# Kernel tuning notes

Hardware: AMD Instinct MI355X
Metric: run time of the kernel (lower is better)

Reference implementation:

```python
import jax, jax.numpy as jnp
import numpy as np

B, N, DIN, DOUT, T, R, H = 4, 384, 128, 128, 4, 4, 8
DK = DOUT // H
SQRT_DK = float(np.sqrt(DK))


def setup_inputs() -> dict:
    key = jax.random.key(0)
    k = jax.random.split(key, 12)
    node_features = jax.random.normal(k[0], (B, N, DIN), jnp.float32)
    nt = jax.random.uniform(k[1], (B, N, T), dtype=jnp.float32)
    node_types_soft = nt / nt.sum(-1, keepdims=True)  # soft type distribution
    adj_matrix_soft = jax.random.uniform(k[2], (B, N, N), dtype=jnp.float32)
    et = jax.random.uniform(k[3], (B, N, N, R), dtype=jnp.float32)
    edge_types_soft = et / et.sum(-1, keepdims=True)  # soft relation distribution
    s = 0.05  # ~xavier scale for 128x128
    return dict(
        node_features=node_features,
        node_types_soft=node_types_soft,
        adj_matrix_soft=adj_matrix_soft,
        edge_types_soft=edge_types_soft,
        kw=jax.random.normal(k[4], (T, DIN, DOUT), jnp.float32) * s,
        kb=jnp.zeros((T, DOUT), jnp.float32),
        qw=jax.random.normal(k[5], (T, DIN, DOUT), jnp.float32) * s,
        qb=jnp.zeros((T, DOUT), jnp.float32),
        vw=jax.random.normal(k[6], (T, DIN, DOUT), jnp.float32) * s,
        vb=jnp.zeros((T, DOUT), jnp.float32),
        aw=jax.random.normal(k[7], (T, DOUT, DOUT), jnp.float32) * s,
        ab=jnp.zeros((T, DOUT), jnp.float32),
        norm_w=jnp.ones((T, DOUT), jnp.float32),
        norm_b=jnp.zeros((T, DOUT), jnp.float32),
        rel_pri=jnp.ones((R, H), jnp.float32),
        rel_att=jax.random.normal(k[8], (R, H, DK, DK), jnp.float32) * 0.1,
        rel_msg=jax.random.normal(k[9], (R, H, DK, DK), jnp.float32) * 0.1,
        skip=jnp.ones((T,), jnp.float32),
    )


def _forward(node_features, node_types_soft, adj_matrix_soft, edge_types_soft,
             kw, kb, qw, qb, vw, vb, aw, ab, norm_w, norm_b,
             rel_pri, rel_att, rel_msg, skip):
    Bq, Nn, _ = node_features.shape
    nt = node_types_soft
    # per-type Q/K/V projections: [B,N,T,H,DK]
    q = (jnp.einsum('bni,tid->bntd', node_features, qw) + qb).reshape(Bq, Nn, T, H, DK)
    kk = (jnp.einsum('bni,tid->bntd', node_features, kw) + kb).reshape(Bq, Nn, T, H, DK)
    v = (jnp.einsum('bni,tid->bntd', node_features, vw) + vb).reshape(Bq, Nn, T, H, DK)

    res_att = jnp.zeros((Bq, Nn, Nn, H), node_features.dtype)
    res_msg = jnp.zeros((Bq, Nn, Nn, H, DK), node_features.dtype)
    for r in range(R):  # small fixed relation count; types/heads fully vectorized
        kr = jnp.einsum('bjshe,hed->bjshd', kk, rel_att[r])
        vr = jnp.einsum('bjshe,hed->bjshd', v, rel_msg[r])
        # fold target-type mask (applied at node j in the original) into k: [B,N,Tt,Ts,H,DK]
        krt = kr[:, :, None] * nt[:, :, :, None, None, None]
        # P[b,i,j,s,h] = sum_{t,d} q[b,i,t,h,d] * nt[b,j,t] * kr[b,j,s,h,d], scaled
        P = jnp.einsum('bithd,bjtshd->bijsh', q, krt) * (rel_pri[r] / SQRT_DK)
        mask = edge_types_soft[..., r] * adj_matrix_soft  # [B,N,N]
        res_att = res_att + jnp.einsum('bijsh,bis->bijh', P, nt) * mask[..., None]
        res_msg = res_msg + jnp.einsum('bijsh,bis,bjshd->bijhd', P, nt, vr) * mask[..., None, None]

    att_sum = res_att.sum(axis=1, keepdims=True)
    safe = jnp.where(att_sum > 1e-6, att_sum, jnp.ones_like(att_sum))
    attw = (res_att / safe) * (att_sum > 1e-6).astype(res_att.dtype)
    agg = jnp.einsum('btsh,btshd->bthd', attw, res_msg).reshape(Bq, Nn, DOUT)

    trans = jnp.einsum('bnd,tdo->bnto', agg, aw) + ab
    trans = jax.nn.gelu(trans, approximate=False)  # dropout = identity at eval
    alpha = jax.nn.sigmoid(skip)[None, None, :, None]
    # in_dim == out_dim -> identity skip projection
    res = trans * alpha + node_features[:, :, None, :] * (1.0 - alpha)
    mean = res.mean(-1, keepdims=True)
    var = res.var(-1, keepdims=True)
    res = (res - mean) / jnp.sqrt(var + 1e-5) * norm_w + norm_b
    return (res * nt[..., None]).sum(axis=2)  # [B,N,DOUT]


def reference(node_features, node_types_soft, adj_matrix_soft, edge_types_soft,
              kw, kb, qw, qb, vw, vb, aw, ab, norm_w, norm_b,
              rel_pri, rel_att, rel_msg, skip):
    return _forward(node_features, node_types_soft, adj_matrix_soft, edge_types_soft,
                    kw, kb, qw, qb, vw, vb, aw, ab, norm_w, norm_b,
                    rel_pri, rel_att, rel_msg, skip)
```

## Files before the change

kernel.cpp:

```cpp
#include <hip/hip_runtime.h>
#include <math.h>

#define Bq 4
#define Nn 384
#define NB 1536
#define TT 4
#define RR 4
#define HH 8
#define DKk 16
#define APART 12288

typedef __attribute__((ext_vector_type(8))) short short8;
typedef __attribute__((ext_vector_type(4))) float f32x4;

__device__ __forceinline__ unsigned short f2bf(float f) {
  unsigned u = __float_as_uint(f);
  u += 0x7FFFu + ((u >> 16) & 1u);
  return (unsigned short)(u >> 16);
}

__device__ __forceinline__ void ld16(const float* __restrict__ p, float* o) {
  const float4* p4 = reinterpret_cast<const float4*>(p);
  float4 a = p4[0], b = p4[1], c = p4[2], d = p4[3];
  o[0]=a.x; o[1]=a.y; o[2]=a.z; o[3]=a.w;
  o[4]=b.x; o[5]=b.y; o[6]=b.z; o[7]=b.w;
  o[8]=c.x; o[9]=c.y; o[10]=c.z; o[11]=c.w;
  o[12]=d.x; o[13]=d.y; o[14]=d.z; o[15]=d.w;
}

__device__ __forceinline__ void bar_lds() {
  asm volatile("s_waitcnt lgkmcnt(0)" ::: "memory");
  __builtin_amdgcn_s_barrier();
}


__global__ __launch_bounds__(256) void k1a_qkv(
    const float* __restrict__ nf,
    const float* __restrict__ qw, const float* __restrict__ qb,
    const float* __restrict__ kw, const float* __restrict__ kb,
    const float* __restrict__ vw, const float* __restrict__ vb,
    float* __restrict__ q_ws, float* __restrict__ kv_k, float* __restrict__ kv_v)
{
  __shared__ float A_s[32][72];
  __shared__ float W_s[32][132];
  int mt = blockIdx.x, t = blockIdx.y, z = blockIdx.z;
  const float* W    = (z == 0) ? qw : ((z == 1) ? kw : vw);
  const float* bias = (z == 0) ? qb : ((z == 1) ? kb : vb);
  int tid = threadIdx.x;
  int colq = (tid & 31)*4, n8 = (tid >> 5)*8;
  float acc[8][4];
#pragma unroll
  for (int u = 0; u < 8; ++u)
#pragma unroll
    for (int c = 0; c < 4; ++c) acc[u][c] = 0.f;

  for (int kc = 0; kc < 4; ++kc) {
    __syncthreads();
    {
      int kk = tid & 31, nb0 = tid >> 5;
#pragma unroll
      for (int u = 0; u < 8; ++u)
        A_s[kk][nb0 + u*8] = nf[(size_t)(mt*64 + nb0 + u*8)*128 + kc*32 + kk];
#pragma unroll
      for (int u = 0; u < 4; ++u) {
        int idx = u*256 + tid;
        int wk = idx >> 5, c4 = (idx & 31)*4;
        *(float4*)&W_s[wk][c4] = *(const float4*)&W[(size_t)(t*128 + kc*32 + wk)*128 + c4];
      }
    }
    __syncthreads();
#pragma unroll
    for (int k = 0; k < 32; ++k) {
      float4 w4 = *(float4*)&W_s[k][colq];
      float a0[8];
      *(float4*)&a0[0] = *(float4*)&A_s[k][n8];
      *(float4*)&a0[4] = *(float4*)&A_s[k][n8 + 4];
#pragma unroll
      for (int u = 0; u < 8; ++u) {
        acc[u][0] += a0[u]*w4.x; acc[u][1] += a0[u]*w4.y;
        acc[u][2] += a0[u]*w4.z; acc[u][3] += a0[u]*w4.w;
      }
    }
  }
  float4 bv = *(const float4*)&bias[t*128 + colq];
#pragma unroll
  for (int u = 0; u < 8; ++u) {
    int node = mt*64 + n8 + u;
    float4 o;
    o.x = acc[u][0] + bv.x; o.y = acc[u][1] + bv.y;
    o.z = acc[u][2] + bv.z; o.w = acc[u][3] + bv.w;
    if (z == 0) {
      int h = colq >> 4, d = colq & 15;
      *(float4*)&q_ws[((size_t)h*NB + node)*64 + t*16 + d] = o;
    } else {
      float* dst = (z == 1) ? kv_k : kv_v;
      *(float4*)&dst[(size_t)node*512 + t*128 + colq] = o;
    }
  }
}

__global__ __launch_bounds__(256) void k1b_rel(
    const float* __restrict__ kv_k, const float* __restrict__ kv_v,
    const float* __restrict__ rel_att, const float* __restrict__ rel_msg,
    float* __restrict__ kr_ws, float* __restrict__ vr_ws,
    float* __restrict__ agg, float* __restrict__ out)
{
  __shared__ float ra_s[4][16][16];
  __shared__ float rm_s[4][16][16];
  __shared__ float k_s[16][4][17];
  __shared__ float v_s[16][4][17];
  int nb = blockIdx.x, h = blockIdx.y;
  int n0 = nb*16;
  int tid = threadIdx.x;
  agg[(size_t)(n0 + (tid >> 4))*128 + h*16 + (tid & 15)] = 0.f;
  out[(size_t)(n0 + (tid >> 4))*128 + h*16 + (tid & 15)] = 0.f;
#pragma unroll
  for (int u0 = 0; u0 < 4; ++u0) {
    int u = u0*256 + tid;
    int r = u >> 8, e = (u >> 4) & 15, d = u & 15;
    ra_s[r][e][d] = rel_att[((size_t)(r*8 + h)*16 + e)*16 + d];
    rm_s[r][e][d] = rel_msg[((size_t)(r*8 + h)*16 + e)*16 + d];
    int nl = u >> 6, s = (u >> 4) & 3, e2 = u & 15;
    k_s[nl][s][e2] = kv_k[(size_t)(n0 + nl)*512 + s*128 + h*16 + e2];
    v_s[nl][s][e2] = kv_v[(size_t)(n0 + nl)*512 + s*128 + h*16 + e2];
  }
  __syncthreads();
  int nl = tid >> 4, dq = tid & 15;
  size_t obase = ((size_t)h*NB + n0 + nl)*256;
#pragma unroll
  for (int r = 0; r < 4; ++r)
#pragma unroll
    for (int s = 0; s < 4; ++s) {
      float aK = 0.f, aV = 0.f;
#pragma unroll
      for (int e = 0; e < 16; ++e) {
        aK += k_s[nl][s][e] * ra_s[r][e][dq];
        aV += v_s[nl][s][e] * rm_s[r][e][dq];
      }
      kr_ws[obase + r*64 + s*16 + dq] = aK;
      vr_ws[obase + r*64 + s*16 + dq] = aV;
    }
}

__global__ __launch_bounds__(256,2) void k2_att(
    const float* __restrict__ nt, const float* __restrict__ adj,
    const float* __restrict__ ets, const float* __restrict__ rel_pri,
    const float* __restrict__ q_ws, const float* __restrict__ kr_ws,
    float* __restrict__ res_att, float* __restrict__ att_part)
{
  __shared__ float q_s[16*68];
  __shared__ float kr_s[32*260];
  __shared__ float ntj_s[32*4];
  int bx = blockIdx.x, h = blockIdx.y, b = blockIdx.z;
  int it = bx >> 1, jh = bx & 1;
  int i0 = it*16;
  int tid = threadIdx.x;
  int j_l = tid>>3, ig = (tid>>1)&3, dh = tid&1;
  {
    int i = tid>>4, f = (tid&15)*4;
    float4 qv = *(const float4*)&q_ws[((size_t)(h*NB) + b*Nn + i0 + i)*64 + f];
    *(float4*)&q_s[i*68 + f] = qv;
  }
  float ntiv[4][4];
#pragma unroll
  for (int il = 0; il < 4; ++il) {
    float4 v = *(const float4*)&nt[(size_t)(b*Nn + i0 + ig*4 + il)*TT];
    ntiv[il][0]=v.x; ntiv[il][1]=v.y; ntiv[il][2]=v.z; ntiv[il][3]=v.w;
  }
  float crr[4];
#pragma unroll
  for (int r = 0; r < 4; ++r) crr[r] = rel_pri[r*HH+h]*0.25f;

  for (int jc = jh*6; jc < jh*6 + 6; ++jc) {
    __syncthreads();
    {
      int js = tid>>3, gb = tid&7;
      const float* src = &kr_ws[((size_t)(h*NB) + b*Nn + jc*32 + js)*256];
      float* dst = &kr_s[js*260];
#pragma unroll
      for (int gl = 0; gl < 8; ++gl) {
        int g = gl*8 + gb;
        *(float4*)&dst[g*4] = *(const float4*)&src[g*4];
      }
      if (tid < 128) ntj_s[tid] = nt[(size_t)(b*Nn + jc*32 + (tid>>2))*TT + (tid&3)];
    }
    __syncthreads();
    int j = jc*32 + j_l;
    float nt0 = ntj_s[j_l*4+0], nt1 = ntj_s[j_l*4+1];
    float nt2 = ntj_s[j_l*4+2], nt3 = ntj_s[j_l*4+3];
    float qn[4][8];
#pragma unroll
    for (int il = 0; il < 4; ++il) {
      const float* qb2 = &q_s[(ig*4 + il)*68 + dh*8];
      float4 a0 = *(const float4*)&qb2[0],  a1 = *(const float4*)&qb2[4];
      float4 b0 = *(const float4*)&qb2[16], b1 = *(const float4*)&qb2[20];
      float4 c0 = *(const float4*)&qb2[32], c1 = *(const float4*)&qb2[36];
      float4 d0v = *(const float4*)&qb2[48], d1v = *(const float4*)&qb2[52];
      qn[il][0] = a0.x*nt0 + b0.x*nt1 + c0.x*nt2 + d0v.x*nt3;
      qn[il][1] = a0.y*nt0 + b0.y*nt1 + c0.y*nt2 + d0v.y*nt3;
      qn[il][2] = a0.z*nt0 + b0.z*nt1 + c0.z*nt2 + d0v.z*nt3;
      qn[il][3] = a0.w*nt0 + b0.w*nt1 + c0.w*nt2 + d0v.w*nt3;
      qn[il][4] = a1.x*nt0 + b1.x*nt1 + c1.x*nt2 + d1v.x*nt3;
      qn[il][5] = a1.y*nt0 + b1.y*nt1 + c1.y*nt2 + d1v.y*nt3;
      qn[il][6] = a1.z*nt0 + b1.z*nt1 + c1.z*nt2 + d1v.z*nt3;
      qn[il][7] = a1.w*nt0 + b1.w*nt1 + c1.w*nt2 + d1v.w*nt3;
    }
    float mar[4][4];
#pragma unroll
    for (int il = 0; il < 4; ++il) {
      int i = i0 + ig*4 + il;
      float a = adj[((size_t)b*Nn + i)*Nn + j];
      float4 e4 = *(const float4*)&ets[(((size_t)b*Nn + i)*Nn + j)*RR];
      mar[il][0]=e4.x*a; mar[il][1]=e4.y*a; mar[il][2]=e4.z*a; mar[il][3]=e4.w*a;
    }
    float acc[4] = {0.f,0.f,0.f,0.f};
    const float* kbp = &kr_s[j_l*260 + dh*8];
#pragma unroll
    for (int r = 0; r < 4; ++r) {
      float mr0 = mar[0][r]*crr[r], mr1 = mar[1][r]*crr[r];
      float mr2 = mar[2][r]*crr[r], mr3 = mar[3][r]*crr[r];
#pragma unroll
      for (int s = 0; s < 4; ++s) {
        float kk[8];
        *(float4*)&kk[0] = *(const float4*)&kbp[r*64 + s*16];
        *(float4*)&kk[4] = *(const float4*)&kbp[r*64 + s*16 + 4];
        float d0=0,d1=0,d2=0,d3=0;
#pragma unroll
        for (int dp = 0; dp < 8; ++dp) {
          d0 += qn[0][dp]*kk[dp]; d1 += qn[1][dp]*kk[dp];
          d2 += qn[2][dp]*kk[dp]; d3 += qn[3][dp]*kk[dp];
        }
        acc[0] += mr0*ntiv[0][s]*d0;
        acc[1] += mr1*ntiv[1][s]*d1;
        acc[2] += mr2*ntiv[2][s]*d2;
        acc[3] += mr3*ntiv[3][s]*d3;
      }
    }
#pragma unroll
    for (int il = 0; il < 4; ++il)
      acc[il] += __shfl_xor(acc[il], 1);
    if (dh == 0) {
#pragma unroll
      for (int il = 0; il < 4; ++il)
        res_att[((size_t)(b*HH + h)*Nn + i0 + ig*4 + il)*Nn + j] = acc[il];
    }
    float v = acc[0] + acc[1] + acc[2] + acc[3];
    v += __shfl_xor(v, 2);
    v += __shfl_xor(v, 4);
    if ((tid & 7) == 0)
      att_part[(size_t)it*APART + (size_t)(b*HH + h)*Nn + j] = v;
  }
}

__global__ __launch_bounds__(256) void kc_agg(
    const float* __restrict__ nt, const float* __restrict__ adj,
    const float* __restrict__ ets, const float* __restrict__ rel_pri,
    const float* __restrict__ q_ws, const float* __restrict__ kr_ws,
    const float* __restrict__ vr_ws, const float* __restrict__ res_att,
    const float* __restrict__ att_part, float* __restrict__ agg)
{
  __shared__ __align__(16) unsigned short B_lds[4][64*72];
  __shared__ __align__(16) unsigned short vr_lds[64*72];
  __shared__ __align__(16) unsigned short Z_lds[4][16*72];
  __shared__ float ntj_s[256];
  __shared__ float inv_s[64];
  int it = blockIdx.x, jc = blockIdx.y, bh = blockIdx.z;
  int b = bh >> 3, h = bh & 7;
  int tid = threadIdx.x, w = tid >> 6, l = tid & 63;
  int j0 = jc*64;
  int ib = it*64 + w*16;
  int irow = ib + (l & 15);
  int iz = ib + ((l >> 4) << 2);
  int lq = (l >> 4) * 8;
  ntj_s[tid] = nt[(size_t)(b*Nn + j0 + (tid>>2))*4 + (tid&3)];
  if (tid < 64) {
    float s = 0.f;
#pragma unroll
    for (int p = 0; p < 24; ++p)
      s += att_part[(size_t)p*APART + (size_t)bh*Nn + j0 + tid];
    inv_s[tid] = (s > 1e-6f) ? 1.f/s : 0.f;
  }
  short8 af[4][2];
  {
    float q0[8], q1[8];
    const float* qp = &q_ws[((size_t)h*NB + b*Nn + irow)*64];
    *(float4*)&q0[0] = *(const float4*)&qp[lq];
    *(float4*)&q0[4] = *(const float4*)&qp[lq + 4];
    *(float4*)&q1[0] = *(const float4*)&qp[32 + lq];
    *(float4*)&q1[4] = *(const float4*)&qp[32 + lq + 4];
    float4 ntiv = *(const float4*)&nt[(size_t)(b*Nn + irow)*4];
    float nta[4] = {ntiv.x, ntiv.y, ntiv.z, ntiv.w};
#pragma unroll
    for (int s = 0; s < 4; ++s)
#pragma unroll
      for (int e = 0; e < 8; ++e) {
        af[s][0][e] = (short)f2bf(q0[e]*nta[s]);
        af[s][1][e] = (short)f2bf(q1[e]*nta[s]);
      }
  }
  float crv[4];
#pragma unroll
  for (int r = 0; r < 4; ++r) crv[r] = rel_pri[r*HH + h]*0.25f;
  float cw[4][4];
  int eo[4][4];
  const float* ebase = ets + (size_t)b*Nn*Nn*4;
#pragma unroll
  for (int tj = 0; tj < 4; ++tj) {
    int j = j0 + tj*16 + (l & 15);
#pragma unroll
    for (int p = 0; p < 4; ++p) {
      int i = iz + p;
      cw[tj][p] = res_att[((size_t)bh*Nn + i)*Nn + j]
                * adj[((size_t)b*Nn + i)*Nn + j];
      eo[tj][p] = (i*Nn + j)*4;
    }
  }
  f32x4 agg_acc = {0.f,0.f,0.f,0.f};
  int js = tid >> 2, ss = tid & 3;
  const float* krp = &kr_ws[((size_t)h*NB + b*Nn + j0 + js)*256 + ss*16];
  const float* vrp = &vr_ws[((size_t)h*NB + b*Nn + j0 + js)*256 + ss*16];
  float kvA[16], vvA[16];
  ld16(krp, kvA);
  ld16(vrp, vvA);
  bar_lds();
#pragma unroll
  for (int tj = 0; tj < 4; ++tj) {
    float inv = inv_s[tj*16 + (l & 15)];
#pragma unroll
    for (int p = 0; p < 4; ++p) cw[tj][p] *= inv;
  }

#pragma unroll
  for (int r = 0; r < 4; ++r) {
    if (r) bar_lds();
    {
      float crr = crv[r];
      float4 ntjv = *(const float4*)&ntj_s[js*4];
      float nta[4] = {ntjv.x*crr, ntjv.y*crr, ntjv.z*crr, ntjv.w*crr};
#pragma unroll
      for (int t = 0; t < 4; ++t) {
#pragma unroll
        for (int dq = 0; dq < 2; ++dq) {
          short8 v;
#pragma unroll
          for (int e = 0; e < 8; ++e) v[e] = (short)f2bf(kvA[dq*8 + e]*nta[t]);
          *(short8*)&B_lds[ss][js*72 + t*16 + dq*8] = v;
        }
      }
#pragma unroll
      for (int d = 0; d < 16; ++d)
        vr_lds[(ss*16 + d)*72 + js] = f2bf(vvA[d]);
    }
    float kvB[16], vvB[16];
    if (r < 3) {
      ld16(krp + (r+1)*64, kvB);
      ld16(vrp + (r+1)*64, vvB);
    }
    bar_lds();
    float coef[4][4];
#pragma unroll
    for (int tj = 0; tj < 4; ++tj)
#pragma unroll
      for (int p = 0; p < 4; ++p)
        coef[tj][p] = ebase[eo[tj][p] + r] * cw[tj][p];
#pragma unroll
    for (int s = 0; s < 4; ++s) {
      f32x4 wacc[4];
#pragma unroll
      for (int tj = 0; tj < 4; ++tj) wacc[tj] = (f32x4){0.f,0.f,0.f,0.f};
#pragma unroll
      for (int tj = 0; tj < 4; ++tj) {
        short8 b0 = *(const short8*)&B_lds[s][(tj*16 + (l & 15))*72 + lq];
        short8 b1 = *(const short8*)&B_lds[s][(tj*16 + (l & 15))*72 + 32 + lq];
        wacc[tj] = __builtin_amdgcn_mfma_f32_16x16x32_bf16(af[s][0], b0, wacc[tj], 0, 0, 0);
        wacc[tj] = __builtin_amdgcn_mfma_f32_16x16x32_bf16(af[s][1], b1, wacc[tj], 0, 0, 0);
      }
#pragma unroll
      for (int tj = 0; tj < 4; ++tj)
#pragma unroll
        for (int p = 0; p < 4; ++p)
          Z_lds[w][(((l >> 4)*4) + p)*72 + tj*16 + (l & 15)] = f2bf(wacc[tj][p]*coef[tj][p]);
#pragma unroll
      for (int kj = 0; kj < 2; ++kj) {
        short8 zf = *(const short8*)&Z_lds[w][(l & 15)*72 + kj*32 + lq];
        short8 vf = *(const short8*)&vr_lds[(s*16 + (l & 15))*72 + kj*32 + lq];
        agg_acc = __builtin_amdgcn_mfma_f32_16x16x32_bf16(zf, vf, agg_acc, 0, 0, 0);
      }
    }
    if (r < 3) {
#pragma unroll
      for (int e = 0; e < 16; ++e) { kvA[e] = kvB[e]; vvA[e] = vvB[e]; }
    }
  }
#pragma unroll
  for (int p = 0; p < 4; ++p)
    atomicAdd(&agg[((size_t)b*Nn + iz + p)*128 + h*16 + (l & 15)], agg_acc[p]);
}

__global__ __launch_bounds__(128) void k5_out(
    const float* __restrict__ agg_ws, const float* __restrict__ nf,
    const float* __restrict__ nt, const float* __restrict__ aw,
    const float* __restrict__ ab, const float* __restrict__ norm_w,
    const float* __restrict__ norm_b, const float* __restrict__ skip,
    float* __restrict__ out)
{
  __shared__ float agg_s[4][128];
  int nq = blockIdx.x, t = blockIdx.y;
  int tid = threadIdx.x;
  int g = tid >> 5, o0 = (tid & 31)*4;
  {
    int nl = tid >> 5, c = (tid & 31)*4;
    *(float4*)&agg_s[nl][c] = *(const float4*)&agg_ws[(size_t)(nq*4 + nl)*128 + c];
  }
  __syncthreads();
  size_t node = (size_t)nq*4 + g;
  float alpha = 1.f/(1.f + expf(-skip[t]));
  float4 bv = *(const float4*)&ab[t*128 + o0];
  float a0 = bv.x, a1 = bv.y, a2 = bv.z, a3 = bv.w;
  const float* awt = aw + (size_t)t*128*128;
  for (int dd = 0; dd < 128; ++dd) {
    float av = agg_s[g][dd];
    float4 wv = *(const float4*)&awt[dd*128 + o0];
    a0 += av*wv.x; a1 += av*wv.y; a2 += av*wv.z; a3 += av*wv.w;
  }
  float4 nfv = *(const float4*)&nf[node*128 + o0];
  float av4[4] = {a0, a1, a2, a3};
  float nfa[4] = {nfv.x, nfv.y, nfv.z, nfv.w};
  float res[4];
#pragma unroll
  for (int c = 0; c < 4; ++c) {
    float gl = 0.5f*av4[c]*(1.f + erff(av4[c]*0.70710678118654752f));
    res[c] = gl*alpha + nfa[c]*(1.f - alpha);
  }
  float s1 = res[0]+res[1]+res[2]+res[3];
  float s2 = res[0]*res[0]+res[1]*res[1]+res[2]*res[2]+res[3]*res[3];
#pragma unroll
  for (int m = 16; m >= 1; m >>= 1) { s1 += __shfl_xor(s1, m); s2 += __shfl_xor(s2, m); }
  float mean = s1*(1.f/128.f);
  float var  = s2*(1.f/128.f) - mean*mean;
  float rstd = rsqrtf(var + 1e-5f);
  float ntv = nt[node*TT + t];
  float4 nwv = *(const float4*)&norm_w[t*128 + o0];
  float4 nbv = *(const float4*)&norm_b[t*128 + o0];
  float nww[4] = {nwv.x, nwv.y, nwv.z, nwv.w};
  float nbb[4] = {nbv.x, nbv.y, nbv.z, nbv.w};
#pragma unroll
  for (int c = 0; c < 4; ++c) {
    float nrm = (res[c] - mean)*rstd*nww[c] + nbb[c];
    atomicAdd(&out[node*128 + o0 + c], nrm*ntv);
  }
}

extern "C" void kernel_launch(void* const* d_in, const int* in_sizes, int n_in,
                              void* d_out, int out_size, void* d_ws, size_t ws_size,
                              hipStream_t stream) {
  const float* nf      = (const float*)d_in[0];
  const float* nts     = (const float*)d_in[1];
  const float* adj     = (const float*)d_in[2];
  const float* ets     = (const float*)d_in[3];
  const float* kw      = (const float*)d_in[4];
  const float* kb      = (const float*)d_in[5];
  const float* qw      = (const float*)d_in[6];
  const float* qb      = (const float*)d_in[7];
  const float* vw      = (const float*)d_in[8];
  const float* vb      = (const float*)d_in[9];
  const float* aw      = (const float*)d_in[10];
  const float* ab      = (const float*)d_in[11];
  const float* normw   = (const float*)d_in[12];
  const float* normb   = (const float*)d_in[13];
  const float* rel_pri = (const float*)d_in[14];
  const float* rel_att = (const float*)d_in[15];
  const float* rel_msg = (const float*)d_in[16];
  const float* skip    = (const float*)d_in[17];
  (void)in_sizes; (void)n_in; (void)out_size; (void)ws_size;

  float* ws = (float*)d_ws;
  float* q_ws    = ws;
  float* kr_ws   = q_ws + 786432;
  float* vr_ws   = kr_ws + 3145728;
  float* res_att = vr_ws + 3145728;
  float* att_part= res_att + 4718592;
  float* agg_ws  = att_part + 294912 + 12288;
  float* kv_k = res_att;
  float* kv_v = res_att + 786432;

  hipLaunchKernelGGL(k1a_qkv, dim3(24, 4, 3), dim3(256), 0, stream,
                     nf, qw, qb, kw, kb, vw, vb, q_ws, kv_k, kv_v);
  hipLaunchKernelGGL(k1b_rel, dim3(96, 8), dim3(256), 0, stream,
                     kv_k, kv_v, rel_att, rel_msg, kr_ws, vr_ws, agg_ws, (float*)d_out);
  hipLaunchKernelGGL(k2_att, dim3(48, 8, 4), dim3(256), 0, stream,
                     nts, adj, ets, rel_pri, q_ws, kr_ws, res_att, att_part);
  hipLaunchKernelGGL(kc_agg, dim3(6, 6, 32), dim3(256), 0, stream,
                     nts, adj, ets, rel_pri, q_ws, kr_ws, vr_ws, res_att, att_part, agg_ws);
  hipLaunchKernelGGL(k5_out, dim3(384, 4), dim3(128), 0, stream,
                     agg_ws, nf, nts, aw, ab, normw, normb, skip, (float*)d_out);
}
```

Measured before the change: 184.0 us.

## Double kc_agg block to 128 rows and split K/V staging across thread halves

The aggregation kernel now uses 512-thread blocks, each covering 128 query rows instead of 64. This halves the grid and lets each staged 64-column K/V tile in LDS be reused by twice as many rows. The K staging work is given to the first 256 threads and the V staging work to the second 256, so each thread holds half as many prefetch registers. The per-j node-type values now come straight from global memory instead of through an LDS array. The catch is fewer, larger blocks, a bigger LDS footprint for Z, and divergent staging branches that could lower occupancy or tail utilisation.

New measurement: 212.5 us. 1.15x slower.

```diff
diff --git a/kernel.cpp b/kernel.cpp
--- a/kernel.cpp
+++ b/kernel.cpp
@@ -252,7 +252,7 @@
   }
 }
 
-__global__ __launch_bounds__(256) void kc_agg(
+__global__ __launch_bounds__(512, 4) void kc_agg(
     const float* __restrict__ nt, const float* __restrict__ adj,
     const float* __restrict__ ets, const float* __restrict__ rel_pri,
     const float* __restrict__ q_ws, const float* __restrict__ kr_ws,
@@ -261,18 +261,16 @@
 {
   __shared__ __align__(16) unsigned short B_lds[4][64*72];
   __shared__ __align__(16) unsigned short vr_lds[64*72];
-  __shared__ __align__(16) unsigned short Z_lds[4][16*72];
-  __shared__ float ntj_s[256];
+  __shared__ __align__(16) unsigned short Z_lds[8][16*72];
   __shared__ float inv_s[64];
   int it = blockIdx.x, jc = blockIdx.y, bh = blockIdx.z;
   int b = bh >> 3, h = bh & 7;
   int tid = threadIdx.x, w = tid >> 6, l = tid & 63;
   int j0 = jc*64;
-  int ib = it*64 + w*16;
+  int ib = it*128 + w*16;
   int irow = ib + (l & 15);
   int iz = ib + ((l >> 4) << 2);
   int lq = (l >> 4) * 8;
-  ntj_s[tid] = nt[(size_t)(b*Nn + j0 + (tid>>2))*4 + (tid&3)];
   if (tid < 64) {
     float s = 0.f;
 #pragma unroll
@@ -316,12 +314,14 @@
     }
   }
   f32x4 agg_acc = {0.f,0.f,0.f,0.f};
-  int js = tid >> 2, ss = tid & 3;
-  const float* krp = &kr_ws[((size_t)h*NB + b*Nn + j0 + js)*256 + ss*16];
-  const float* vrp = &vr_ws[((size_t)h*NB + b*Nn + j0 + js)*256 + ss*16];
-  float kvA[16], vvA[16];
-  ld16(krp, kvA);
-  ld16(vrp, vvA);
+  int sj = (tid & 255) >> 2, ss = tid & 3;
+  bool doB = (tid < 256);
+  const float* srcp = doB
+      ? &kr_ws[((size_t)h*NB + b*Nn + j0 + sj)*256 + ss*16]
+      : &vr_ws[((size_t)h*NB + b*Nn + j0 + sj)*256 + ss*16];
+  float vA[16];
+  ld16(srcp, vA);
+  float4 ntjv = *(const float4*)&nt[(size_t)(b*Nn + j0 + sj)*4];
   bar_lds();
 #pragma unroll
   for (int tj = 0; tj < 4; ++tj) {
@@ -333,9 +333,8 @@
 #pragma unroll
   for (int r = 0; r < 4; ++r) {
     if (r) bar_lds();
-    {
+    if (doB) {
       float crr = crv[r];
-      float4 ntjv = *(const float4*)&ntj_s[js*4];
       float nta[4] = {ntjv.x*crr, ntjv.y*crr, ntjv.z*crr, ntjv.w*crr};
 #pragma unroll
       for (int t = 0; t < 4; ++t) {
@@ -343,19 +342,17 @@
         for (int dq = 0; dq < 2; ++dq) {
           short8 v;
 #pragma unroll
-          for (int e = 0; e < 8; ++e) v[e] = (short)f2bf(kvA[dq*8 + e]*nta[t]);
-          *(short8*)&B_lds[ss][js*72 + t*16 + dq*8] = v;
+          for (int e = 0; e < 8; ++e) v[e] = (short)f2bf(vA[dq*8 + e]*nta[t]);
+          *(short8*)&B_lds[ss][sj*72 + t*16 + dq*8] = v;
         }
       }
+    } else {
 #pragma unroll
       for (int d = 0; d < 16; ++d)
-        vr_lds[(ss*16 + d)*72 + js] = f2bf(vvA[d]);
-    }
-    float kvB[16], vvB[16];
-    if (r < 3) {
-      ld16(krp + (r+1)*64, kvB);
-      ld16(vrp + (r+1)*64, vvB);
-    }
+        vr_lds[(ss*16 + d)*72 + sj] = f2bf(vA[d]);
+    }
+    float vB[16];
+    if (r < 3) ld16(srcp + (r+1)*64, vB);
     bar_lds();
     float coef[4][4];
 #pragma unroll
@@ -389,7 +386,7 @@
     }
     if (r < 3) {
 #pragma unroll
-      for (int e = 0; e < 16; ++e) { kvA[e] = kvB[e]; vvA[e] = vvB[e]; }
+      for (int e = 0; e < 16; ++e) vA[e] = vB[e];
     }
   }
 #pragma unroll
@@ -490,7 +487,7 @@
                      kv_k, kv_v, rel_att, rel_msg, kr_ws, vr_ws, agg_ws, (float*)d_out);
   hipLaunchKernelGGL(k2_att, dim3(48, 8, 4), dim3(256), 0, stream,
                      nts, adj, ets, rel_pri, q_ws, kr_ws, res_att, att_part);
-  hipLaunchKernelGGL(kc_agg, dim3(6, 6, 32), dim3(256), 0, stream,
+  hipLaunchKernelGGL(kc_agg, dim3(3, 6, 32), dim3(512), 0, stream,
                      nts, adj, ets, rel_pri, q_ws, kr_ws, vr_ws, res_att, att_part, agg_ws);
   hipLaunchKernelGGL(k5_out, dim3(384, 4), dim3(128), 0, stream,
                      agg_ws, nf, nts, aw, ab, normw, normb, skip, (float*)d_out);
```

## Split k2_att key staging into two relation halves and use three j-segments

Applied to the files above, without the earlier changes.

The attention kernel now stages the relation-transformed keys in shared memory in two halves (relations 0-1, then 2-3) instead of all at once, roughly halving the kr_s tile. The j range per block is cut into three segments of four chunks instead of two of six, raising the grid from 48 to 72 blocks in x. The aim is higher occupancy and more parallelism for this kernel, at the cost of extra __syncthreads and a second shared-memory staging pass per chunk.

Result: slower. 197.4 us (+7.2%).

```diff
diff --git a/kernel.cpp b/kernel.cpp
--- a/kernel.cpp
+++ b/kernel.cpp
@@ -149,10 +149,10 @@
     float* __restrict__ res_att, float* __restrict__ att_part)
 {
   __shared__ float q_s[16*68];
-  __shared__ float kr_s[32*260];
+  __shared__ float kr_s[32*132];
   __shared__ float ntj_s[32*4];
   int bx = blockIdx.x, h = blockIdx.y, b = blockIdx.z;
-  int it = bx >> 1, jh = bx & 1;
+  int it = bx / 3, jseg = bx % 3;
   int i0 = it*16;
   int tid = threadIdx.x;
   int j_l = tid>>3, ig = (tid>>1)&3, dh = tid&1;
@@ -171,14 +171,14 @@
 #pragma unroll
   for (int r = 0; r < 4; ++r) crr[r] = rel_pri[r*HH+h]*0.25f;
 
-  for (int jc = jh*6; jc < jh*6 + 6; ++jc) {
+  int js = tid>>3, gb = tid&7;
+  for (int jc = jseg*4; jc < jseg*4 + 4; ++jc) {
     __syncthreads();
+    const float* src = &kr_ws[((size_t)(h*NB) + b*Nn + jc*32 + js)*256];
     {
-      int js = tid>>3, gb = tid&7;
-      const float* src = &kr_ws[((size_t)(h*NB) + b*Nn + jc*32 + js)*256];
-      float* dst = &kr_s[js*260];
-#pragma unroll
-      for (int gl = 0; gl < 8; ++gl) {
+      float* dst = &kr_s[js*132];
+#pragma unroll
+      for (int gl = 0; gl < 4; ++gl) {
         int g = gl*8 + gb;
         *(float4*)&dst[g*4] = *(const float4*)&src[g*4];
       }
@@ -214,9 +214,9 @@
       mar[il][0]=e4.x*a; mar[il][1]=e4.y*a; mar[il][2]=e4.z*a; mar[il][3]=e4.w*a;
     }
     float acc[4] = {0.f,0.f,0.f,0.f};
-    const float* kbp = &kr_s[j_l*260 + dh*8];
-#pragma unroll
-    for (int r = 0; r < 4; ++r) {
+    const float* kbp = &kr_s[j_l*132 + dh*8];
+#pragma unroll
+    for (int r = 0; r < 2; ++r) {
       float mr0 = mar[0][r]*crr[r], mr1 = mar[1][r]*crr[r];
       float mr2 = mar[2][r]*crr[r], mr3 = mar[3][r]*crr[r];
 #pragma unroll
@@ -224,6 +224,38 @@
         float kk[8];
         *(float4*)&kk[0] = *(const float4*)&kbp[r*64 + s*16];
         *(float4*)&kk[4] = *(const float4*)&kbp[r*64 + s*16 + 4];
+        float d0=0,d1=0,d2=0,d3=0;
+#pragma unroll
+        for (int dp = 0; dp < 8; ++dp) {
+          d0 += qn[0][dp]*kk[dp]; d1 += qn[1][dp]*kk[dp];
+          d2 += qn[2][dp]*kk[dp]; d3 += qn[3][dp]*kk[dp];
+        }
+        acc[0] += mr0*ntiv[0][s]*d0;
+        acc[1] += mr1*ntiv[1][s]*d1;
+        acc[2] += mr2*ntiv[2][s]*d2;
+        acc[3] += mr3*ntiv[3][s]*d3;
+      }
+    }
+    __syncthreads();
+    {
+      float* dst = &kr_s[js*132];
+#pragma unroll
+      for (int gl = 0; gl < 4; ++gl) {
+        int g = gl*8 + gb;
+        *(float4*)&dst[g*4] = *(const float4*)&src[128 + g*4];
+      }
+    }
+    __syncthreads();
+#pragma unroll
+    for (int r = 2; r < 4; ++r) {
+      int rl = r - 2;
+      float mr0 = mar[0][r]*crr[r], mr1 = mar[1][r]*crr[r];
+      float mr2 = mar[2][r]*crr[r], mr3 = mar[3][r]*crr[r];
+#pragma unroll
+      for (int s = 0; s < 4; ++s) {
+        float kk[8];
+        *(float4*)&kk[0] = *(const float4*)&kbp[rl*64 + s*16];
+        *(float4*)&kk[4] = *(const float4*)&kbp[rl*64 + s*16 + 4];
         float d0=0,d1=0,d2=0,d3=0;
 #pragma unroll
         for (int dp = 0; dp < 8; ++dp) {
@@ -488,7 +520,7 @@
                      nf, qw, qb, kw, kb, vw, vb, q_ws, kv_k, kv_v);
   hipLaunchKernelGGL(k1b_rel, dim3(96, 8), dim3(256), 0, stream,
                      kv_k, kv_v, rel_att, rel_msg, kr_ws, vr_ws, agg_ws, (float*)d_out);
-  hipLaunchKernelGGL(k2_att, dim3(48, 8, 4), dim3(256), 0, stream,
+  hipLaunchKernelGGL(k2_att, dim3(72, 8, 4), dim3(256), 0, stream,
                      nts, adj, ets, rel_pri, q_ws, kr_ws, res_att, att_part);
   hipLaunchKernelGGL(kc_agg, dim3(6, 6, 32), dim3(256), 0, stream,
                      nts, adj, ets, rel_pri, q_ws, kr_ws, vr_ws, res_att, att_part, agg_ws);
```
